# Performance work log

Measured on AMD Instinct MI355X. Metric: run time of the kernel, lower is better.

## Reference

```python
import jax, jax.numpy as jnp
import numpy as np

B, D, H, K = 16384, 512, 4, 128  # batch, d_model, num_heads, key_dim=d_model//4
EPS = 1e-6


def _layernorm(x, gamma, beta):
    mean = jnp.mean(x, axis=-1, keepdims=True)
    var = jnp.mean(jnp.square(x - mean), axis=-1, keepdims=True)
    return gamma * (x - mean) / jnp.sqrt(var + EPS) + beta


def setup_inputs() -> dict:
    key = jax.random.key(0)
    ks = jax.random.split(key, 32)
    n = lambda i, shape, s=0.02: jax.random.normal(ks[i], shape, jnp.float32) * s
    inp = {
        'frontier': n(0, (B, D), 1.0),
        'cross_robot': n(1, (B, D), 1.0),
        'map_feat': n(2, (B, D), 1.0),
        # three input projections
        'Wf': n(3, (D, D)), 'bf': n(4, (D,), 0.01),
        'Wr': n(5, (D, D)), 'br': n(6, (D,), 0.01),
        'Wm': n(7, (D, D)), 'bm': n(8, (D,), 0.01),
        # adaptive weight MLP: 3D -> D//2 -> 3 (softmax)
        'Wa1': n(9, (3 * D, D // 2)), 'ba1': n(10, (D // 2,), 0.01),
        'Wa2': n(11, (D // 2, 3)), 'ba2': n(12, (3,), 0.01),
        # multi-head attention (keras MHA layout)
        'Wq': n(13, (D, H, K)), 'bq': n(14, (H, K), 0.01),
        'Wk': n(15, (D, H, K)), 'bk': n(16, (H, K), 0.01),
        'Wv': n(17, (D, H, K)), 'bv': n(18, (H, K), 0.01),
        'Wo': n(19, (H, K, D)), 'bo': n(20, (D,), 0.01),
        # sigmoid gate
        'Wg': n(21, (D, D)), 'bg': n(22, (D,), 0.01),
        # two custom layernorms
        'gamma1': jnp.ones((D,), jnp.float32), 'beta1': jnp.zeros((D,), jnp.float32),
        'gamma2': jnp.ones((D,), jnp.float32), 'beta2': jnp.zeros((D,), jnp.float32),
    }
    return inp


def reference(frontier, cross_robot, map_feat, Wf, bf, Wr, br, Wm, bm,
              Wa1, ba1, Wa2, ba2, Wq, bq, Wk, bk, Wv, bv, Wo, bo,
              Wg, bg, gamma1, beta1, gamma2, beta2):
    # projections [B, D]
    fp = frontier @ Wf + bf
    rp = cross_robot @ Wr + br
    mp = map_feat @ Wm + bm
    # adaptive softmax weights over the 3 modalities: [B, 3]
    concat = jnp.concatenate([fp, rp, mp], axis=-1)
    h = jax.nn.relu(concat @ Wa1 + ba1)
    aw = jax.nn.softmax(h @ Wa2 + ba2, axis=-1)
    # length-3 sequence self-attention (keras MultiHeadAttention, dropout off)
    x = jnp.stack([fp, rp, mp], axis=1)  # [B, 3, D]
    q = jnp.einsum('bsd,dhk->bshk', x, Wq) + bq
    k = jnp.einsum('bsd,dhk->bshk', x, Wk) + bk
    v = jnp.einsum('bsd,dhk->bshk', x, Wv) + bv
    scores = jnp.einsum('bqhk,bshk->bhqs', q, k) / jnp.sqrt(jnp.float32(K))
    attn = jax.nn.softmax(scores, axis=-1)  # [B, H, 3, 3]
    ctx = jnp.einsum('bhqs,bshk->bqhk', attn, v)
    o = jnp.einsum('bqhk,hkd->bqd', ctx, Wo) + bo  # [B, 3, D]
    y = _layernorm(x + o, gamma1, beta1)  # residual + LN1
    # adaptive weighted combination of the 3 attended modalities
    weighted = jnp.einsum('bs,bsd->bd', aw, y)  # [B, D]
    gate = jax.nn.sigmoid(weighted @ Wg + bg)
    out = _layernorm(mp + gate * weighted, gamma2, beta2)
    return out
```

## Files before the change

### kernel.cpp

```cpp
#include <hip/hip_runtime.h>
#include <math.h>

#define BATCH 16384L
#define WSZ   (512L * 512)
#define PLANE (BATCH * 512)
#define SEGBIG (1L << 40)
#define DTF(dtp) ((*(dtp)) == 0x3F800000u)

typedef __bf16 bf16_t;
typedef bf16_t bf16x8 __attribute__((ext_vector_type(8)));
typedef float f32x4 __attribute__((ext_vector_type(4)));

struct Srcs { const void* A[3]; const void* bias[3]; };
struct Ptr8 { const void* p[8]; };

__device__ __forceinline__ float ldf(const void* p, long i, int dtf) {
  return dtf ? ((const float*)p)[i] : (float)((const bf16_t*)p)[i];
}
__device__ __forceinline__ bf16x8 ld8(const void* p, long i, int dtf) {
  if (dtf) {
    const float* f = (const float*)p + i;
    f32x4 a = *(const f32x4*)f, b = *(const f32x4*)(f + 4);
    bf16x8 r;
#pragma unroll
    for (int j = 0; j < 4; j++) { r[j] = (bf16_t)a[j]; r[4 + j] = (bf16_t)b[j]; }
    return r;
  }
  return *(const bf16x8*)((const bf16_t*)p + i);
}
__device__ __forceinline__ void ld8f(const void* p, long i, int dtf, float* o) {
  if (dtf) {
    const float* f = (const float*)p + i;
    f32x4 a = *(const f32x4*)f, b = *(const f32x4*)(f + 4);
#pragma unroll
    for (int j = 0; j < 4; j++) { o[j] = a[j]; o[4 + j] = b[j]; }
  } else {
    bf16x8 v = *(const bf16x8*)((const bf16_t*)p + i);
#pragma unroll
    for (int j = 0; j < 8; j++) o[j] = (float)v[j];
  }
}

__global__ __launch_bounds__(256) void gemm_bt(
    Srcs S, int lda, long segRows, long segStride, long termStride, int aExt,
    const bf16_t* __restrict__ WT0, int ldw, long zStrW, int wTermOff,
    bf16_t* __restrict__ C0, int ldc, long zStrC,
    int nterms, int act, int biasShift, const unsigned* __restrict__ dtp)
{
  __shared__ bf16_t lA[2][128 * 32];
  __shared__ bf16_t lB[2][128 * 32];
  const int isf  = DTF(dtp);
  const int z    = blockIdx.z;
  const void* A  = S.A[z];
  const int adtf = aExt & isf;
  const bf16_t* WT = WT0 + (long)z * zStrW;
  bf16_t* C = C0 + (long)z * zStrC;

  const int tid = threadIdx.x, wave = tid >> 6, lane = tid & 63;
  const long rowBase = (long)blockIdx.x * 128;
  const long colBase = (long)blockIdx.y * 128;
  const long aBase = (rowBase / segRows) * segStride + (rowBase % segRows) * (long)lda;

  const int r0 = tid >> 2, cc = (tid & 3) << 3;
  const int arow = ((wave & 1) << 6) + (lane & 15);
  const int brow = ((wave >> 1) << 6) + (lane & 15);
  const int koff = (lane >> 4) << 3;
  const int niter = nterms << 4;

#define LOADIT(it, A0, A1, B0, B1) {                                      \
    int t_ = (it) >> 4; long k0_ = (long)(((it) & 15) << 5) + cc;         \
    long aT_ = aBase + (long)t_ * termStride + k0_;                       \
    A0 = ld8(A, aT_ + (long)r0 * lda, adtf);                              \
    A1 = ld8(A, aT_ + (long)(64 + r0) * lda, adtf);                       \
    const bf16_t* Wt_ = WT + (long)t_ * wTermOff + k0_;                   \
    B0 = *(const bf16x8*)(Wt_ + (colBase + r0) * (long)ldw);              \
    B1 = *(const bf16x8*)(Wt_ + (colBase + 64 + r0) * (long)ldw); }
#define WRITEB(bf, A0, A1, B0, B1) {                                      \
    *(bf16x8*)(lA[bf] + r0 * 32 + cc) = A0;                               \
    *(bf16x8*)(lA[bf] + (64 + r0) * 32 + cc) = A1;                        \
    *(bf16x8*)(lB[bf] + r0 * 32 + cc) = B0;                               \
    *(bf16x8*)(lB[bf] + (64 + r0) * 32 + cc) = B1; }

  f32x4 acc[4][4];
#pragma unroll
  for (int i = 0; i < 4; i++)
#pragma unroll
    for (int j = 0; j < 4; j++) acc[i][j] = (f32x4){0.f, 0.f, 0.f, 0.f};

  bf16x8 ca0, ca1, cb0, cb1, na0, na1, nb0, nb1;
  LOADIT(0, ca0, ca1, cb0, cb1);
  WRITEB(0, ca0, ca1, cb0, cb1);
  if (niter > 1) LOADIT(1, na0, na1, nb0, nb1);
  __syncthreads();

  for (int k = 0; k < niter; ++k) {
    const int cur = k & 1;
    bf16x8 af[4], bfr[4];
#pragma unroll
    for (int ti = 0; ti < 4; ti++)
      af[ti] = *(const bf16x8*)(lA[cur] + (arow + ti * 16) * 32 + koff);
#pragma unroll
    for (int tj = 0; tj < 4; tj++)
      bfr[tj] = *(const bf16x8*)(lB[cur] + (brow + tj * 16) * 32 + koff);
    if (k + 1 < niter) WRITEB(cur ^ 1, na0, na1, nb0, nb1);
    __syncthreads();
    if (k + 2 < niter) LOADIT(k + 2, na0, na1, nb0, nb1);
#pragma unroll
    for (int ti = 0; ti < 4; ti++)
#pragma unroll
      for (int tj = 0; tj < 4; tj++)
        acc[ti][tj] = __builtin_amdgcn_mfma_f32_16x16x32_bf16(af[ti], bfr[tj], acc[ti][tj], 0, 0, 0);
  }
#undef LOADIT
#undef WRITEB

  const long orow0 = rowBase + ((wave & 1) << 6) + ((lane >> 4) << 2);
  const long ocol0 = colBase + ((wave >> 1) << 6) + (lane & 15);
#pragma unroll
  for (int ti = 0; ti < 4; ti++) {
#pragma unroll
    for (int tj = 0; tj < 4; tj++) {
      long gcol = ocol0 + tj * 16;
      const void* bp = S.bias[z + (int)(gcol >> biasShift)];
      float bv = bp ? ldf(bp, gcol & ((1L << biasShift) - 1), isf) : 0.f;
#pragma unroll
      for (int r = 0; r < 4; r++) {
        long grow = orow0 + ti * 16 + r;
        float v = acc[ti][tj][r] + bv;
        if (act == 1) v = v > 0.f ? v : 0.f;
        else if (act == 2) v = 1.f / (1.f + __expf(-v));
        C[grow * ldc + gcol] = (bf16_t)v;
      }
    }
  }
}

__global__ __launch_bounds__(256) void transpose8(Ptr8 in, bf16_t* __restrict__ out,
                                                  const unsigned* __restrict__ dtp) {
  __shared__ bf16_t tile[32][33];
  const int dtf = DTF(dtp);
  const void* src = in.p[blockIdx.z];
  bf16_t* dst = out + (long)blockIdx.z * WSZ;
  int bc = blockIdx.x * 32, br = blockIdx.y * 32;
  int tx = threadIdx.x & 31, ty = threadIdx.x >> 5;
  for (int i = ty; i < 32; i += 8)
    tile[i][tx] = (bf16_t)ldf(src, (long)(br + i) * 512 + bc + tx, dtf);
  __syncthreads();
  for (int i = ty; i < 32; i += 8) dst[(long)(bc + i) * 512 + br + tx] = tile[tx][i];
}

__global__ __launch_bounds__(256) void transpose_any(const void* __restrict__ in,
                                                     bf16_t* __restrict__ out, int R, int C,
                                                     const unsigned* __restrict__ dtp) {
  __shared__ bf16_t tile[32][33];
  const int dtf = DTF(dtp);
  int bc = blockIdx.x * 32, br = blockIdx.y * 32;
  int tx = threadIdx.x & 31, ty = threadIdx.x >> 5;
  for (int i = ty; i < 32; i += 8)
    tile[i][tx] = (bf16_t)ldf(in, (long)(br + i) * C + bc + tx, dtf);
  __syncthreads();
  for (int i = ty; i < 32; i += 8) out[(long)(bc + i) * R + br + tx] = tile[tx][i];
}

__global__ __launch_bounds__(256) void adaw(const bf16_t* __restrict__ H, long pStr, int np,
                                            const void* __restrict__ ba1,
                                            const void* __restrict__ Wa2,
                                            const void* __restrict__ ba2,
                                            float* __restrict__ aw,
                                            const unsigned* __restrict__ dtp) {
  const int dtf = DTF(dtp);
  long b = (long)blockIdx.x * 256 + threadIdx.x;
  float l0 = ldf(ba2, 0, dtf), l1 = ldf(ba2, 1, dtf), l2 = ldf(ba2, 2, dtf);
  for (int kk = 0; kk < 256; kk += 8) {
    float hv[8];
    bf16x8 h0 = *(const bf16x8*)(H + b * 256 + kk);
#pragma unroll
    for (int j = 0; j < 8; j++) hv[j] = (float)h0[j];
    if (np > 1) {
      bf16x8 h1 = *(const bf16x8*)(H + pStr + b * 256 + kk);
      bf16x8 h2 = *(const bf16x8*)(H + 2 * pStr + b * 256 + kk);
#pragma unroll
      for (int j = 0; j < 8; j++) hv[j] += (float)h1[j] + (float)h2[j];
    }
    float bb[8];
    ld8f(ba1, kk, dtf, bb);
#pragma unroll
    for (int j = 0; j < 8; j++) {
      float x = hv[j] + bb[j];
      x = x > 0.f ? x : 0.f;
      l0 += x * ldf(Wa2, (kk + j) * 3 + 0, dtf);
      l1 += x * ldf(Wa2, (kk + j) * 3 + 1, dtf);
      l2 += x * ldf(Wa2, (kk + j) * 3 + 2, dtf);
    }
  }
  float m = fmaxf(l0, fmaxf(l1, l2));
  float e0 = __expf(l0 - m), e1 = __expf(l1 - m), e2 = __expf(l2 - m);
  float inv = 1.f / (e0 + e1 + e2);
  aw[b * 3 + 0] = e0 * inv;
  aw[b * 3 + 1] = e1 * inv;
  aw[b * 3 + 2] = e2 * inv;
}

__global__ __launch_bounds__(256) void attn_small(bf16_t* __restrict__ QKV, long rs) {
  const int tid = threadIdx.x;
  const int l = tid & 15;
  const int G = tid >> 4;
  const long b = (long)blockIdx.x * 4 + (G >> 2);
  const int h = G & 3;
  const long base = b * 1536 + h * 128 + l * 8;

  bf16x8 q[3], k[3], v[3];
#pragma unroll
  for (int s = 0; s < 3; s++) {
    q[s] = *(const bf16x8*)(QKV + s * rs + base);
    k[s] = *(const bf16x8*)(QKV + s * rs + base + 512);
    v[s] = *(const bf16x8*)(QKV + s * rs + base + 1024);
  }
  float sc[3][3];
#pragma unroll
  for (int s = 0; s < 3; s++)
#pragma unroll
    for (int t = 0; t < 3; t++) {
      float p = 0.f;
#pragma unroll
      for (int j = 0; j < 8; j++) p += (float)q[s][j] * (float)k[t][j];
      p += __shfl_xor(p, 1); p += __shfl_xor(p, 2);
      p += __shfl_xor(p, 4); p += __shfl_xor(p, 8);
      sc[s][t] = p;
    }
  const float scale = 0.088388347648318447f;
  float at[3][3];
#pragma unroll
  for (int qs = 0; qs < 3; qs++) {
    float a0 = sc[qs][0] * scale, a1 = sc[qs][1] * scale, a2 = sc[qs][2] * scale;
    float m = fmaxf(a0, fmaxf(a1, a2));
    float e0 = __expf(a0 - m), e1 = __expf(a1 - m), e2 = __expf(a2 - m);
    float inv = 1.f / (e0 + e1 + e2);
    at[qs][0] = e0 * inv; at[qs][1] = e1 * inv; at[qs][2] = e2 * inv;
  }
#pragma unroll
  for (int s = 0; s < 3; s++) {
    bf16x8 o;
#pragma unroll
    for (int j = 0; j < 8; j++)
      o[j] = (bf16_t)(at[s][0] * (float)v[0][j] + at[s][1] * (float)v[1][j] +
                      at[s][2] * (float)v[2][j]);
    *(bf16x8*)(QKV + s * rs + base) = o;
  }
}

__global__ __launch_bounds__(192) void ln1_weighted(const bf16_t* __restrict__ P,
                                                    const bf16_t* __restrict__ O,
                                                    const float* __restrict__ aw,
                                                    const void* __restrict__ g1,
                                                    const void* __restrict__ b1,
                                                    bf16_t* __restrict__ Wout,
                                                    long bofs, long chunkRows,
                                                    const unsigned* __restrict__ dtp) {
  __shared__ float buf[3 * 512];
  const int dtf = DTF(dtp);
  long bl = blockIdx.x;
  long bg = bofs + bl;
  int wave = threadIdx.x >> 6, lane = threadIdx.x & 63;
  long prow = ((long)wave * BATCH + bg) * 512;
  long orow = ((long)wave * chunkRows + bl) * 512;
  int c0 = lane * 8;
  bf16x8 x8 = *(const bf16x8*)(P + prow + c0);
  bf16x8 o8 = *(const bf16x8*)(O + orow + c0);
  float tv[8], s1 = 0.f, s2 = 0.f;
#pragma unroll
  for (int j = 0; j < 8; j++) {
    float v = (float)x8[j] + (float)o8[j];
    tv[j] = v; s1 += v; s2 += v * v;
  }
  for (int off = 32; off; off >>= 1) { s1 += __shfl_xor(s1, off); s2 += __shfl_xor(s2, off); }
  float mean = s1 * (1.f / 512.f);
  float var = s2 * (1.f / 512.f) - mean * mean;
  float inv = rsqrtf(var + 1e-6f);
  float a = aw[bg * 3 + wave];
  float gv[8], bv[8];
  ld8f(g1, c0, dtf, gv); ld8f(b1, c0, dtf, bv);
#pragma unroll
  for (int j = 0; j < 8; j++)
    buf[wave * 512 + c0 + j] = a * (gv[j] * ((tv[j] - mean) * inv) + bv[j]);
  __syncthreads();
  if (wave == 0) {
    bf16x8 w8;
#pragma unroll
    for (int j = 0; j < 8; j++)
      w8[j] = (bf16_t)(buf[c0 + j] + buf[512 + c0 + j] + buf[1024 + c0 + j]);
    *(bf16x8*)(Wout + bg * 512 + c0) = w8;
  }
}

__global__ __launch_bounds__(256) void ln2_out(const bf16_t* __restrict__ MP,
                                               const bf16_t* __restrict__ G,
                                               const bf16_t* __restrict__ Wt,
                                               const void* __restrict__ g2,
                                               const void* __restrict__ b2,
                                               void* __restrict__ out,
                                               const unsigned* __restrict__ dtp) {
  const int dtf = DTF(dtp);
  int wave = threadIdx.x >> 6, lane = threadIdx.x & 63;
  long b = (long)blockIdx.x * 4 + wave;
  long row = b * 512;
  int c0 = lane * 8;
  bf16x8 m8 = *(const bf16x8*)(MP + row + c0);
  bf16x8 g8 = *(const bf16x8*)(G + row + c0);
  bf16x8 w8 = *(const bf16x8*)(Wt + row + c0);
  float tv[8], s1 = 0.f, s2 = 0.f;
#pragma unroll
  for (int j = 0; j < 8; j++) {
    float v = (float)m8[j] + (float)g8[j] * (float)w8[j];
    tv[j] = v; s1 += v; s2 += v * v;
  }
  for (int off = 32; off; off >>= 1) { s1 += __shfl_xor(s1, off); s2 += __shfl_xor(s2, off); }
  float mean = s1 * (1.f / 512.f);
  float var = s2 * (1.f / 512.f) - mean * mean;
  float inv = rsqrtf(var + 1e-6f);
  float gv[8], bv[8];
  ld8f(g2, c0, dtf, gv); ld8f(b2, c0, dtf, bv);
  if (dtf) {
    f32x4 o0, o1;
#pragma unroll
    for (int j = 0; j < 4; j++) {
      o0[j] = gv[j] * ((tv[j] - mean) * inv) + bv[j];
      o1[j] = gv[4 + j] * ((tv[4 + j] - mean) * inv) + bv[4 + j];
    }
    *(f32x4*)((float*)out + row + c0) = o0;
    *(f32x4*)((float*)out + row + c0 + 4) = o1;
  } else {
    bf16x8 r8;
#pragma unroll
    for (int j = 0; j < 8; j++)
      r8[j] = (bf16_t)(gv[j] * ((tv[j] - mean) * inv) + bv[j]);
    *(bf16x8*)((bf16_t*)out + row + c0) = r8;
  }
}

extern "C" void kernel_launch(void* const* d_in, const int* in_sizes, int n_in,
                              void* d_out, int out_size, void* d_ws, size_t ws_size,
                              hipStream_t stream) {
  const void* frontier = d_in[0];
  const void* cross    = d_in[1];
  const void* mapf     = d_in[2];
  const void* Wf  = d_in[3];  const void* bf_  = d_in[4];
  const void* Wr  = d_in[5];  const void* br_  = d_in[6];
  const void* Wm  = d_in[7];  const void* bm_  = d_in[8];
  const void* Wa1 = d_in[9];  const void* ba1  = d_in[10];
  const void* Wa2 = d_in[11]; const void* ba2  = d_in[12];
  const void* Wq  = d_in[13]; const void* bq   = d_in[14];
  const void* Wk  = d_in[15]; const void* bk   = d_in[16];
  const void* Wv  = d_in[17]; const void* bv   = d_in[18];
  const void* Wo  = d_in[19]; const void* bo   = d_in[20];
  const void* Wg  = d_in[21]; const void* bg   = d_in[22];
  const void* gamma1 = d_in[23]; const void* beta1 = d_in[24];
  const void* gamma2 = d_in[25]; const void* beta2 = d_in[26];
  const unsigned* dtp = (const unsigned*)gamma1;

  bf16_t* WTb  = (bf16_t*)d_ws;
  bf16_t* Wa1T = WTb + 8 * WSZ;
  bf16_t* P    = Wa1T + 256L * 1536;
  float*  AW   = (float*)(P + 3 * PLANE);
  char*   region = (char*)(AW + 3 * BATCH);
  long avail = (long)ws_size - (long)(region - (char*)d_ws);

  int adaSplit = avail >= 3 * BATCH * 256 * 2;
  long BC = BATCH;
  while (BC > 512 && 12288L * BC > avail) BC >>= 1;

  bf16_t* Hp   = (bf16_t*)region;
  bf16_t* QKVc = (bf16_t*)region;
  bf16_t* Oc   = QKVc + 3 * BC * 1536;
  bf16_t* WTd  = P;
  bf16_t* GT   = P + PLANE;

  Ptr8 w8 = {{Wf, Wr, Wm, Wq, Wk, Wv, Wo, Wg}};
  transpose8<<<dim3(16, 16, 8), 256, 0, stream>>>(w8, WTb, dtp);
  transpose_any<<<dim3(8, 48), 256, 0, stream>>>(Wa1, Wa1T, 1536, 256, dtp);

  Srcs sp = {{frontier, cross, mapf}, {bf_, br_, bm_}};
  gemm_bt<<<dim3(128, 4, 3), 256, 0, stream>>>(sp, 512, SEGBIG, 0, 0, 1,
      WTb, 512, WSZ, 0, P, 512, PLANE, 1, 0, 30, dtp);

  if (adaSplit) {
    Srcs sa = {{P, P + PLANE, P + 2 * PLANE}, {nullptr, nullptr, nullptr}};
    gemm_bt<<<dim3(128, 2, 3), 256, 0, stream>>>(sa, 512, SEGBIG, 0, 0, 0,
        Wa1T, 1536, 512, 0, Hp, 256, BATCH * 256, 1, 0, 30, dtp);
    adaw<<<dim3(BATCH / 256), 256, 0, stream>>>(Hp, BATCH * 256, 3, ba1, Wa2, ba2, AW, dtp);
  } else {
    Srcs sa = {{P, nullptr, nullptr}, {nullptr, nullptr, nullptr}};
    gemm_bt<<<dim3(128, 2, 1), 256, 0, stream>>>(sa, 512, SEGBIG, 0, PLANE, 0,
        Wa1T, 1536, 0, 512, Hp, 256, 0, 3, 0, 30, dtp);
    adaw<<<dim3(BATCH / 256), 256, 0, stream>>>(Hp, 0, 1, ba1, Wa2, ba2, AW, dtp);
  }

  for (long c = 0; c < BATCH / BC; ++c) {
    Srcs sq = {{P + c * BC * 512, nullptr, nullptr}, {bq, bk, bv}};
    gemm_bt<<<dim3((unsigned)(3 * BC / 128), 12, 1), 256, 0, stream>>>(sq,
        512, BC, PLANE, 0, 0, WTb + 3 * WSZ, 512, 0, 0, QKVc, 1536, 0, 1, 0, 9, dtp);
    attn_small<<<dim3((unsigned)(BC / 4)), 256, 0, stream>>>(QKVc, BC * 1536);
    Srcs so = {{QKVc, nullptr, nullptr}, {bo, nullptr, nullptr}};
    gemm_bt<<<dim3((unsigned)(3 * BC / 128), 4, 1), 256, 0, stream>>>(so,
        1536, SEGBIG, 0, 0, 0, WTb + 6 * WSZ, 512, 0, 0, Oc, 512, 0, 1, 0, 30, dtp);
    ln1_weighted<<<dim3((unsigned)BC), dim3(192), 0, stream>>>(P, Oc, AW,
        gamma1, beta1, WTd, c * BC, BC, dtp);
  }

  Srcs sg = {{WTd, nullptr, nullptr}, {bg, nullptr, nullptr}};
  gemm_bt<<<dim3(128, 4, 1), 256, 0, stream>>>(sg, 512, SEGBIG, 0, 0, 0,
      WTb + 7 * WSZ, 512, 0, 0, GT, 512, 0, 1, 2, 30, dtp);

  ln2_out<<<dim3(BATCH / 4), 256, 0, stream>>>(P + 2 * PLANE, GT, WTd,
      gamma2, beta2, d_out, dtp);
}
```

Baseline: 610.3 us.

## Load GEMM tiles directly into LDS with global_load_lds, single-buffered

Replaces the register-staged double-buffered LDS tile loading in the bf16 GEMM with direct global-to-LDS loads (global_load_lds, 16 bytes per lane) for the weight tile and for bf16 activations. The fp32 activation path still converts through registers, prefetched one iteration ahead. LDS shrinks to a single buffer and each iteration now needs two barriers, so the loads no longer overlap the MFMA work of the previous tile. This removes register pressure and VGPR round-trips but gives up the software pipelining.

```diff
diff --git a/kernel.cpp b/kernel.cpp
--- a/kernel.cpp
+++ b/kernel.cpp
@@ -13,6 +13,12 @@
 
 struct Srcs { const void* A[3]; const void* bias[3]; };
 struct Ptr8 { const void* p[8]; };
+
+__device__ __forceinline__ void glds16(const bf16_t* g, bf16_t* l) {
+  __builtin_amdgcn_global_load_lds((const __attribute__((address_space(1))) void*)g,
+                                   (__attribute__((address_space(3))) void*)l,
+                                   16, 0, 0);
+}
 
 __device__ __forceinline__ float ldf(const void* p, long i, int dtf) {
   return dtf ? ((const float*)p)[i] : (float)((const bf16_t*)p)[i];
@@ -47,12 +53,13 @@
     bf16_t* __restrict__ C0, int ldc, long zStrC,
     int nterms, int act, int biasShift, const unsigned* __restrict__ dtp)
 {
-  __shared__ bf16_t lA[2][128 * 32];
-  __shared__ bf16_t lB[2][128 * 32];
+  __shared__ bf16_t lA[128 * 32];
+  __shared__ bf16_t lB[128 * 32];
   const int isf  = DTF(dtp);
   const int z    = blockIdx.z;
   const void* A  = S.A[z];
   const int adtf = aExt & isf;
+  const bf16_t* Ab = (const bf16_t*)A;
   const bf16_t* WT = WT0 + (long)z * zStrW;
   bf16_t* C = C0 + (long)z * zStrC;
 
@@ -61,58 +68,65 @@
   const long colBase = (long)blockIdx.y * 128;
   const long aBase = (rowBase / segRows) * segStride + (rowBase % segRows) * (long)lda;
 
-  const int r0 = tid >> 2, cc = (tid & 3) << 3;
+  const int sr = (wave << 4) + (lane >> 2);
+  const int sc = (lane & 3) << 3;
+  bf16_t* ldsA0 = lA + (wave << 4) * 32;
+  bf16_t* ldsA1 = lA + (64 + (wave << 4)) * 32;
+  bf16_t* ldsB0 = lB + (wave << 4) * 32;
+  bf16_t* ldsB1 = lB + (64 + (wave << 4)) * 32;
+
   const int arow = ((wave & 1) << 6) + (lane & 15);
   const int brow = ((wave >> 1) << 6) + (lane & 15);
   const int koff = (lane >> 4) << 3;
   const int niter = nterms << 4;
 
-#define LOADIT(it, A0, A1, B0, B1) {                                      \
-    int t_ = (it) >> 4; long k0_ = (long)(((it) & 15) << 5) + cc;         \
-    long aT_ = aBase + (long)t_ * termStride + k0_;                       \
-    A0 = ld8(A, aT_ + (long)r0 * lda, adtf);                              \
-    A1 = ld8(A, aT_ + (long)(64 + r0) * lda, adtf);                       \
-    const bf16_t* Wt_ = WT + (long)t_ * wTermOff + k0_;                   \
-    B0 = *(const bf16x8*)(Wt_ + (colBase + r0) * (long)ldw);              \
-    B1 = *(const bf16x8*)(Wt_ + (colBase + 64 + r0) * (long)ldw); }
-#define WRITEB(bf, A0, A1, B0, B1) {                                      \
-    *(bf16x8*)(lA[bf] + r0 * 32 + cc) = A0;                               \
-    *(bf16x8*)(lA[bf] + (64 + r0) * 32 + cc) = A1;                        \
-    *(bf16x8*)(lB[bf] + r0 * 32 + cc) = B0;                               \
-    *(bf16x8*)(lB[bf] + (64 + r0) * 32 + cc) = B1; }
-
   f32x4 acc[4][4];
 #pragma unroll
   for (int i = 0; i < 4; i++)
 #pragma unroll
     for (int j = 0; j < 4; j++) acc[i][j] = (f32x4){0.f, 0.f, 0.f, 0.f};
 
-  bf16x8 ca0, ca1, cb0, cb1, na0, na1, nb0, nb1;
-  LOADIT(0, ca0, ca1, cb0, cb1);
-  WRITEB(0, ca0, ca1, cb0, cb1);
-  if (niter > 1) LOADIT(1, na0, na1, nb0, nb1);
-  __syncthreads();
+  bf16x8 ra0, ra1;
+  if (adtf) {
+    ra0 = ld8(A, aBase + (long)sr * lda + sc, 1);
+    ra1 = ld8(A, aBase + (long)(64 + sr) * lda + sc, 1);
+  }
 
   for (int k = 0; k < niter; ++k) {
-    const int cur = k & 1;
+    const int t = k >> 4;
+    const long k0 = (long)((k & 15) << 5) + sc;
+    const long aOfs = aBase + (long)t * termStride + k0;
+    const bf16_t* Wt = WT + (long)t * wTermOff + k0;
+    if (adtf) {
+      *(bf16x8*)(lA + sr * 32 + sc) = ra0;
+      *(bf16x8*)(lA + (64 + sr) * 32 + sc) = ra1;
+    } else {
+      glds16(Ab + aOfs + (long)sr * lda, ldsA0);
+      glds16(Ab + aOfs + (long)(64 + sr) * lda, ldsA1);
+    }
+    glds16(Wt + (colBase + sr) * (long)ldw, ldsB0);
+    glds16(Wt + (colBase + 64 + sr) * (long)ldw, ldsB1);
+    __syncthreads();
     bf16x8 af[4], bfr[4];
 #pragma unroll
     for (int ti = 0; ti < 4; ti++)
-      af[ti] = *(const bf16x8*)(lA[cur] + (arow + ti * 16) * 32 + koff);
+      af[ti] = *(const bf16x8*)(lA + (arow + ti * 16) * 32 + koff);
 #pragma unroll
     for (int tj = 0; tj < 4; tj++)
-      bfr[tj] = *(const bf16x8*)(lB[cur] + (brow + tj * 16) * 32 + koff);
-    if (k + 1 < niter) WRITEB(cur ^ 1, na0, na1, nb0, nb1);
-    __syncthreads();
-    if (k + 2 < niter) LOADIT(k + 2, na0, na1, nb0, nb1);
+      bfr[tj] = *(const bf16x8*)(lB + (brow + tj * 16) * 32 + koff);
+    if (adtf && k + 1 < niter) {
+      const int t2 = (k + 1) >> 4;
+      const long a2 = aBase + (long)t2 * termStride + (long)(((k + 1) & 15) << 5) + sc;
+      ra0 = ld8(A, a2 + (long)sr * lda, 1);
+      ra1 = ld8(A, a2 + (long)(64 + sr) * lda, 1);
+    }
 #pragma unroll
     for (int ti = 0; ti < 4; ti++)
 #pragma unroll
       for (int tj = 0; tj < 4; tj++)
         acc[ti][tj] = __builtin_amdgcn_mfma_f32_16x16x32_bf16(af[ti], bfr[tj], acc[ti][tj], 0, 0, 0);
-  }
-#undef LOADIT
-#undef WRITEB
+    __syncthreads();
+  }
 
   const long orow0 = rowBase + ((wave & 1) << 6) + ((lane >> 4) << 2);
   const long ocol0 = colBase + ((wave >> 1) << 6) + (lane & 15);
```

Result: no change. 609.1 us (-0.2%).
